# Kernel optimization log

Hardware: AMD Instinct MI355X
Metric: run time of the kernel (lower is better)

## Reference

```python
import jax, jax.numpy as jnp
import numpy as np

DIM = 768
NUM_SS = 8
INNER = DIM // 4  # s_ratio = 4 -> 192


def setup_inputs() -> dict:
    key = jax.random.key(0)
    ks = jax.random.split(key, 9)
    s = 0.02
    return {
        "x": jax.random.normal(ks[0], (16, 4096, DIM), dtype=jnp.float32),
        "Wq": jax.random.normal(ks[1], (DIM, DIM), dtype=jnp.float32) * s,
        "bq": jax.random.normal(ks[2], (DIM,), dtype=jnp.float32) * s,
        "Wk": jax.random.normal(ks[3], (DIM, NUM_SS * INNER), dtype=jnp.float32) * s,
        "bk": jax.random.normal(ks[4], (NUM_SS * INNER,), dtype=jnp.float32) * s,
        "Wv": jax.random.normal(ks[5], (DIM, DIM), dtype=jnp.float32) * s,
        "bv": jax.random.normal(ks[6], (DIM,), dtype=jnp.float32) * s,
        "Wss_out": jax.random.normal(ks[7], (INNER, DIM), dtype=jnp.float32) * s,
        "bss_out": jax.random.normal(ks[8], (DIM,), dtype=jnp.float32) * s,
    }


def reference(x, Wq, bq, Wk, bk, Wv, bv, Wss_out, bss_out):
    b = x.shape[0]
    ss_tokens = x[:, -NUM_SS:, :]          # [b, S, D]
    reg = x[:, :-NUM_SS, :]                # [b, T, D]
    x_v = reg @ Wv + bv                    # [b, T, D]
    x_q = reg @ Wq + bq                    # [b, T, D]
    x_k = reg @ Wk + bk                    # [b, T, S*I]
    # mean over regular tokens, reshape to one inner vector per ss token
    ss_update_ = jnp.mean(x_k, axis=1).reshape(b, NUM_SS, INNER)
    new_ss = ss_tokens + (ss_update_ @ Wss_out + bss_out)     # [b, S, D]
    scale = jnp.asarray(1.0 / np.sqrt(DIM), x.dtype)
    sim = jnp.einsum('btd,bsd->bts', x_q, new_ss) * scale     # [b, T, S]
    attn = jax.nn.softmax(sim, axis=-1)
    upd = jnp.einsum('bts,bsd->btd', attn, new_ss)            # [b, T, D]
    new_reg = jax.nn.relu(x_v + upd)
    return jnp.concatenate([new_reg, new_ss], axis=1)
```

## Files before the change

kernel.cpp:

```cpp
#include <hip/hip_runtime.h>
#include <hip/hip_bf16.h>

#define B_ 16
#define T_ 4096
#define TREG 4088
#define D_ 768
#define NSS 8
#define INNER_ 192
#define NK 1536

typedef unsigned int u32;
typedef unsigned short u16;
typedef __attribute__((ext_vector_type(8))) short bf16x8;
typedef __attribute__((ext_vector_type(4))) float f32x4;

__device__ __forceinline__ u16 f2bf(float f) {
  union { __hip_bfloat16 h; u16 u; } cv;
  cv.h = __float2bfloat16(f);
  return cv.u;
}

__device__ __forceinline__ void load16_lds(const void* g, void* l) {
  __builtin_amdgcn_global_load_lds(
      (const __attribute__((address_space(1))) u32*)(unsigned long long)g,
      (__attribute__((address_space(3))) u32*)(u32)(unsigned long long)l,
      16, 0, 0);
}

__global__ __launch_bounds__(256) void k_wvt(const float* __restrict__ Wv,
                                             u16* __restrict__ wvT) {
  __shared__ float tile[16][17];
  int tx = threadIdx.x & 15, ty = threadIdx.x >> 4;
  int nb = blockIdx.x * 16, kb = blockIdx.y * 16;
  tile[ty][tx] = Wv[(size_t)(kb + ty) * D_ + nb + tx];
  __syncthreads();
  wvT[(size_t)(nb + ty) * D_ + kb + tx] = f2bf(tile[tx][ty]);
}

template <bool CONV>
__global__ __launch_bounds__(192) void k_conv_mean(const float* __restrict__ x,
                                                   u16* __restrict__ xb,
                                                   float* __restrict__ means) {
  int b = blockIdx.y, tc = blockIdx.x, tid = threadIdx.x;
  const float4* xp = (const float4*)(x + (size_t)(b * T_ + tc * 128) * D_) + tid;
  ushort4* op = nullptr;
  if (CONV) op = ((ushort4*)(xb + (size_t)(b * T_ + tc * 128) * D_)) + tid;
  float s0 = 0, s1 = 0, s2 = 0, s3 = 0;
  int tbase = tc * 128;
  for (int tt = 0; tt < 128; ++tt) {
    float4 v = xp[(size_t)tt * 192];
    if (CONV) {
      ushort4 o;
      o.x = f2bf(v.x); o.y = f2bf(v.y); o.z = f2bf(v.z); o.w = f2bf(v.w);
      op[(size_t)tt * 192] = o;
    }
    if (tbase + tt < TREG) { s0 += v.x; s1 += v.y; s2 += v.z; s3 += v.w; }
  }
  float* m = means + (size_t)b * D_ + tid * 4;
  atomicAdd(m + 0, s0); atomicAdd(m + 1, s1);
  atomicAdd(m + 2, s2); atomicAdd(m + 3, s3);
}

__global__ __launch_bounds__(256) void k_ssu(const float* __restrict__ means,
                                             const float* __restrict__ Wk,
                                             const float* __restrict__ bk,
                                             float* __restrict__ ssu) {
  int b = blockIdx.y, tid = threadIdx.x;
  int n = blockIdx.x * 256 + tid;
  __shared__ float mv[D_];
  for (int d = tid; d < D_; d += 256)
    mv[d] = means[(size_t)b * D_ + d] * (1.0f / TREG);
  __syncthreads();
  float a = bk[n];
#pragma unroll 8
  for (int d = 0; d < D_; ++d) a += mv[d] * Wk[(size_t)d * NK + n];
  ssu[(size_t)b * NK + n] = a;
}

__global__ __launch_bounds__(256) void k_nss(
    const float* __restrict__ x, const float* __restrict__ ssu,
    const float* __restrict__ Wss, const float* __restrict__ bss,
    const float* __restrict__ bq, float* __restrict__ out,
    float* __restrict__ nssf, u16* __restrict__ nssT, float* __restrict__ qb) {
  int s = blockIdx.x, b = blockIdx.y, tid = threadIdx.x;
  __shared__ float su[INNER_];
  __shared__ float qred[4];
  if (tid < INNER_) su[tid] = ssu[(size_t)b * NK + s * INNER_ + tid];
  __syncthreads();
  size_t xr = (size_t)(b * T_ + TREG + s) * D_;
  float a0 = x[xr + tid]       + bss[tid];
  float a1 = x[xr + tid + 256] + bss[tid + 256];
  float a2 = x[xr + tid + 512] + bss[tid + 512];
#pragma unroll 4
  for (int i = 0; i < INNER_; ++i) {
    float sv = su[i];
    const float* wr = Wss + (size_t)i * D_ + tid;
    a0 += sv * wr[0]; a1 += sv * wr[256]; a2 += sv * wr[512];
  }
  out[xr + tid] = a0; out[xr + tid + 256] = a1; out[xr + tid + 512] = a2;
  size_t nb = (size_t)(b * NSS + s) * D_;
  nssf[nb + tid] = a0; nssf[nb + tid + 256] = a1; nssf[nb + tid + 512] = a2;
  size_t tb = (size_t)b * D_;
  nssT[(tb + tid) * NSS + s] = f2bf(a0);
  nssT[(tb + tid + 256) * NSS + s] = f2bf(a1);
  nssT[(tb + tid + 512) * NSS + s] = f2bf(a2);
  float q = bq[tid] * a0 + bq[tid + 256] * a1 + bq[tid + 512] * a2;
#pragma unroll
  for (int o = 1; o < 64; o <<= 1) q += __shfl_xor(q, o, 64);
  if ((tid & 63) == 0) qred[tid >> 6] = q;
  __syncthreads();
  if (tid == 0) qb[b * NSS + s] = qred[0] + qred[1] + qred[2] + qred[3];
}

__global__ __launch_bounds__(256) void k_wqs(const float* __restrict__ Wq,
                                             const float* __restrict__ nssf,
                                             u16* __restrict__ wqsT) {
  __shared__ float nss[NSS * (D_ + 4)];
  int b = blockIdx.y, tid = threadIdx.x;
  int o = blockIdx.x * 256 + tid;
  int j = o >> 3, s = o & 7;
  for (int i = tid; i < NSS * D_; i += 256) {
    int s2 = i / D_, d2 = i - s2 * D_;
    nss[s2 * (D_ + 4) + d2] = nssf[(size_t)b * NSS * D_ + i];
  }
  __syncthreads();
  const float* wr = Wq + (size_t)j * D_;
  const float* nr = nss + s * (D_ + 4);
  float a = 0;
#pragma unroll 8
  for (int d = 0; d < D_; ++d) a += wr[d] * nr[d];
  wqsT[((size_t)b * NSS + s) * D_ + j] = f2bf(a);
}

template <bool ABF16>
__global__ __launch_bounds__(256) void k_main(
    const u16* __restrict__ xb, const float* __restrict__ xf,
    const u16* __restrict__ wvT, const u16* __restrict__ wqsT,
    const u16* __restrict__ nssTg, const float* __restrict__ qb,
    const float* __restrict__ bv, float* __restrict__ out) {
  __shared__ uint4 ldsv[1800];
  u16* lds = (u16*)ldsv;
  u16* As = lds;
  u16* Bs = lds + 4096;
  u16* Ws = lds + 8192;

  const int tid = threadIdx.x;
  const int b = blockIdx.z;
  const int t0 = blockIdx.y * 128, n0 = blockIdx.x * 128;
  const int wave = tid >> 6, lane = tid & 63;
  const int wy = wave >> 1, wx = wave & 1;
  const int lr = lane & 15, lq = lane >> 4;

  if (tid < 96) {
    for (int s = 0; s < 8; ++s)
      ((uint4*)(Ws + s * 776))[tid] =
          ((const uint4*)(wqsT + ((size_t)b * NSS + s) * D_))[tid];
  }

  f32x4 acc[4][4];
  f32x4 sacc[4];
#pragma unroll
  for (int i = 0; i < 4; ++i) {
    sacc[i] = f32x4{0.f, 0.f, 0.f, 0.f};
#pragma unroll
    for (int j = 0; j < 4; ++j) acc[i][j] = f32x4{0.f, 0.f, 0.f, 0.f};
  }

  const u16* Bg = wvT + (size_t)n0 * D_;
  const int c1 = tid + 256;
  const int ar0 = tid >> 2, ak0 = (tid & 3) * 8;
  const int ar1 = c1 >> 2, ak1 = (c1 & 3) * 8;

  for (int k0 = 0; k0 < D_; k0 += 32) {
    if constexpr (ABF16) {
      const u16* Ag = xb + (size_t)(b * T_ + t0) * D_;
      load16_lds(Ag + (size_t)ar0 * D_ + k0 + ak0, As + tid * 8);
      load16_lds(Ag + (size_t)ar1 * D_ + k0 + ak1, As + c1 * 8);
    } else {
      const float* Af = xf + (size_t)(b * T_ + t0) * D_;
      const float* p0 = Af + (size_t)ar0 * D_ + k0 + ak0;
      const float* p1 = Af + (size_t)ar1 * D_ + k0 + ak1;
      float4 a0 = *(const float4*)p0, a1 = *(const float4*)(p0 + 4);
      float4 a2 = *(const float4*)p1, a3 = *(const float4*)(p1 + 4);
      ushort4 w0, w1, w2, w3;
      w0.x = f2bf(a0.x); w0.y = f2bf(a0.y); w0.z = f2bf(a0.z); w0.w = f2bf(a0.w);
      w1.x = f2bf(a1.x); w1.y = f2bf(a1.y); w1.z = f2bf(a1.z); w1.w = f2bf(a1.w);
      w2.x = f2bf(a2.x); w2.y = f2bf(a2.y); w2.z = f2bf(a2.z); w2.w = f2bf(a2.w);
      w3.x = f2bf(a3.x); w3.y = f2bf(a3.y); w3.z = f2bf(a3.z); w3.w = f2bf(a3.w);
      *(ushort4*)(As + tid * 8) = w0; *(ushort4*)(As + tid * 8 + 4) = w1;
      *(ushort4*)(As + c1 * 8) = w2; *(ushort4*)(As + c1 * 8 + 4) = w3;
    }
    load16_lds(Bg + (size_t)ar0 * D_ + k0 + ak0, Bs + tid * 8);
    load16_lds(Bg + (size_t)ar1 * D_ + k0 + ak1, Bs + c1 * 8);
    __syncthreads();

    bf16x8 af[4], bfr[4], qf;
#pragma unroll
    for (int mt = 0; mt < 4; ++mt)
      af[mt] = *(const bf16x8*)(As + (wy * 64 + mt * 16 + lr) * 32 + lq * 8);
#pragma unroll
    for (int nt = 0; nt < 4; ++nt)
      bfr[nt] = *(const bf16x8*)(Bs + (wx * 64 + nt * 16 + lr) * 32 + lq * 8);
    qf = *(const bf16x8*)(Ws + (lr & 7) * 776 + k0 + lq * 8);
#pragma unroll
    for (int mt = 0; mt < 4; ++mt) {
#pragma unroll
      for (int nt = 0; nt < 4; ++nt)
        acc[mt][nt] = __builtin_amdgcn_mfma_f32_16x16x32_bf16(
            af[mt], bfr[nt], acc[mt][nt], 0, 0, 0);
      sacc[mt] = __builtin_amdgcn_mfma_f32_16x16x32_bf16(
          af[mt], qf, sacc[mt], 0, 0, 0);
    }
    __syncthreads();
  }

  u16* anb = lds;
  u16* nsl = lds + 4096;
  {
    uint4 z; z.x = z.y = z.z = z.w = 0;
    if (tid < 128) {
      uint4 v = *(const uint4*)(nssTg + ((size_t)b * D_ + n0 + tid) * NSS);
      *(uint4*)(nsl + tid * 32) = v;
      *(uint4*)(nsl + tid * 32 + 8) = z;
      *(uint4*)(nsl + tid * 32 + 16) = z;
      *(uint4*)(nsl + tid * 32 + 24) = z;
    } else {
      int r = tid - 128;
      *(uint4*)(anb + r * 32 + 8) = z;
      *(uint4*)(anb + r * 32 + 16) = z;
      *(uint4*)(anb + r * 32 + 24) = z;
    }
  }
  __syncthreads();

  const float scale = 0.03608439182435161f;
  const float qbias = (lr < 8) ? qb[b * NSS + lr] : 0.f;
#pragma unroll
  for (int mt = 0; mt < 4; ++mt) {
    f32x4 s4 = sacc[mt];
#pragma unroll
    for (int r = 0; r < 4; ++r) {
      float v = (lr < 8) ? (s4[r] + qbias) * scale : -1.0e30f;
      float mx = v;
      mx = fmaxf(mx, __shfl_xor(mx, 1, 16));
      mx = fmaxf(mx, __shfl_xor(mx, 2, 16));
      mx = fmaxf(mx, __shfl_xor(mx, 4, 16));
      float e = (lr < 8) ? __expf(v - mx) : 0.f;
      float sm = e;
      sm += __shfl_xor(sm, 1, 16);
      sm += __shfl_xor(sm, 2, 16);
      sm += __shfl_xor(sm, 4, 16);
      if (lr < 8) {
        float a = e / sm;
        anb[(wy * 64 + mt * 16 + lq * 4 + r) * 32 + lr] = f2bf(a);
      }
    }
  }
  __syncthreads();

  bf16x8 nf[4];
#pragma unroll
  for (int nt = 0; nt < 4; ++nt)
    nf[nt] = *(const bf16x8*)(nsl + (wx * 64 + nt * 16 + lr) * 32 + lq * 8);
#pragma unroll
  for (int mt = 0; mt < 4; ++mt) {
    bf16x8 afr = *(const bf16x8*)(anb + (wy * 64 + mt * 16 + lr) * 32 + lq * 8);
#pragma unroll
    for (int nt = 0; nt < 4; ++nt)
      acc[mt][nt] = __builtin_amdgcn_mfma_f32_16x16x32_bf16(
          afr, nf[nt], acc[mt][nt], 0, 0, 0);
  }

  float bvv[4];
#pragma unroll
  for (int nt = 0; nt < 4; ++nt) bvv[nt] = bv[n0 + wx * 64 + nt * 16 + lr];
#pragma unroll
  for (int mt = 0; mt < 4; ++mt) {
    int trow = wy * 64 + mt * 16 + lq * 4;
#pragma unroll
    for (int r = 0; r < 4; ++r) {
      int token = t0 + trow + r;
      if (token < TREG) {
        float* op = out + ((size_t)b * T_ + token) * D_ + n0 + wx * 64;
#pragma unroll
        for (int nt = 0; nt < 4; ++nt)
          op[nt * 16 + lr] = fmaxf(acc[mt][nt][r] + bvv[nt], 0.f);
      }
    }
  }
}

extern "C" void kernel_launch(void* const* d_in, const int* in_sizes, int n_in,
                              void* d_out, int out_size, void* d_ws, size_t ws_size,
                              hipStream_t stream) {
  (void)in_sizes; (void)n_in; (void)out_size;
  const float* x   = (const float*)d_in[0];
  const float* Wq  = (const float*)d_in[1];
  const float* bq  = (const float*)d_in[2];
  const float* Wk  = (const float*)d_in[3];
  const float* bk  = (const float*)d_in[4];
  const float* Wv  = (const float*)d_in[5];
  const float* bv  = (const float*)d_in[6];
  const float* Wss = (const float*)d_in[7];
  const float* bss = (const float*)d_in[8];
  float* out = (float*)d_out;

  const size_t SZ_XB   = (size_t)B_ * T_ * D_ * 2;
  const size_t SZ_WVT  = (size_t)D_ * D_ * 2;
  const size_t SZ_MEAN = (size_t)B_ * D_ * 4;
  const size_t SZ_SSU  = (size_t)B_ * NK * 4;
  const size_t SZ_NSSF = (size_t)B_ * NSS * D_ * 4;
  const size_t SZ_NSST = (size_t)B_ * D_ * NSS * 2;
  const size_t SZ_QB   = (size_t)B_ * NSS * 4;
  const size_t SZ_WQS  = (size_t)B_ * NSS * D_ * 2;
  const size_t SMALL = SZ_WVT + SZ_MEAN + SZ_SSU + SZ_NSSF + SZ_NSST + SZ_QB + SZ_WQS;
  const size_t FULL = SZ_XB + SMALL;
  const bool big = ws_size >= FULL;

  char* ws = (char*)d_ws;
  size_t off = big ? SZ_XB : 0;
  u16*   xb    = (u16*)ws;
  u16*   wvT   = (u16*)(ws + off);   off += SZ_WVT;
  float* means = (float*)(ws + off); off += SZ_MEAN;
  float* ssu   = (float*)(ws + off); off += SZ_SSU;
  float* nssf  = (float*)(ws + off); off += SZ_NSSF;
  u16*   nssT  = (u16*)(ws + off);   off += SZ_NSST;
  float* qbb   = (float*)(ws + off); off += SZ_QB;
  u16*   wqsT  = (u16*)(ws + off);   off += SZ_WQS;

  hipMemsetAsync(means, 0, SZ_MEAN, stream);
  k_wvt<<<dim3(48, 48), 256, 0, stream>>>(Wv, wvT);
  if (big)
    k_conv_mean<true><<<dim3(32, 16), 192, 0, stream>>>(x, xb, means);
  else
    k_conv_mean<false><<<dim3(32, 16), 192, 0, stream>>>(x, nullptr, means);
  k_ssu<<<dim3(6, 16), 256, 0, stream>>>(means, Wk, bk, ssu);
  k_nss<<<dim3(NSS, 16), 256, 0, stream>>>(x, ssu, Wss, bss, bq, out, nssf, nssT, qbb);
  k_wqs<<<dim3(24, 16), 256, 0, stream>>>(Wq, nssf, wqsT);
  if (big)
    k_main<true><<<dim3(6, 32, 16), 256, 0, stream>>>(xb, x, wvT, wqsT, nssT, qbb, bv, out);
  else
    k_main<false><<<dim3(6, 32, 16), 256, 0, stream>>>(nullptr, x, wvT, wqsT, nssT, qbb, bv, out);
}
```

Baseline: 641.0 us.

## Load MFMA fragments directly from global with register prefetch, XCD-aware block swizzle

The main GEMM stops staging the A and B tiles through LDS and instead loads bf16 fragments straight from global memory into registers. It double-buffers them across k-steps and removes the per-iteration barriers. The 1D grid is remapped so that blocks sharing an x tile land on the same XCD for L2 reuse, and launch bounds request 3 blocks per CU with a smaller LDS footprint. The conversion and mean kernel is also split into 4x more blocks for more parallelism, at the cost of 4x more atomics. Direct global fragment loads are less coalesced than LDS staging and raise register pressure.

```diff
diff --git a/kernel.cpp b/kernel.cpp
--- a/kernel.cpp
+++ b/kernel.cpp
@@ -20,13 +20,6 @@
   return cv.u;
 }
 
-__device__ __forceinline__ void load16_lds(const void* g, void* l) {
-  __builtin_amdgcn_global_load_lds(
-      (const __attribute__((address_space(1))) u32*)(unsigned long long)g,
-      (__attribute__((address_space(3))) u32*)(u32)(unsigned long long)l,
-      16, 0, 0);
-}
-
 __global__ __launch_bounds__(256) void k_wvt(const float* __restrict__ Wv,
                                              u16* __restrict__ wvT) {
   __shared__ float tile[16][17];
@@ -42,12 +35,13 @@
                                                    u16* __restrict__ xb,
                                                    float* __restrict__ means) {
   int b = blockIdx.y, tc = blockIdx.x, tid = threadIdx.x;
-  const float4* xp = (const float4*)(x + (size_t)(b * T_ + tc * 128) * D_) + tid;
+  const float4* xp = (const float4*)(x + (size_t)(b * T_ + tc * 32) * D_) + tid;
   ushort4* op = nullptr;
-  if (CONV) op = ((ushort4*)(xb + (size_t)(b * T_ + tc * 128) * D_)) + tid;
+  if (CONV) op = ((ushort4*)(xb + (size_t)(b * T_ + tc * 32) * D_)) + tid;
   float s0 = 0, s1 = 0, s2 = 0, s3 = 0;
-  int tbase = tc * 128;
-  for (int tt = 0; tt < 128; ++tt) {
+  int tbase = tc * 32;
+#pragma unroll 4
+  for (int tt = 0; tt < 32; ++tt) {
     float4 v = xp[(size_t)tt * 192];
     if (CONV) {
       ushort4 o;
@@ -132,21 +126,44 @@
   wqsT[((size_t)b * NSS + s) * D_ + j] = f2bf(a);
 }
 
+template <bool BF>
+__device__ __forceinline__ bf16x8 ldfrag(const u16* pb, const float* pf,
+                                         size_t off) {
+  if constexpr (BF) {
+    return *(const bf16x8*)(pb + off);
+  } else {
+    float4 f0 = *(const float4*)(pf + off);
+    float4 f1 = *(const float4*)(pf + off + 4);
+    bf16x8 r;
+    r[0] = (short)f2bf(f0.x); r[1] = (short)f2bf(f0.y);
+    r[2] = (short)f2bf(f0.z); r[3] = (short)f2bf(f0.w);
+    r[4] = (short)f2bf(f1.x); r[5] = (short)f2bf(f1.y);
+    r[6] = (short)f2bf(f1.z); r[7] = (short)f2bf(f1.w);
+    return r;
+  }
+}
+
 template <bool ABF16>
-__global__ __launch_bounds__(256) void k_main(
+__global__ __launch_bounds__(256, 3) void k_main(
     const u16* __restrict__ xb, const float* __restrict__ xf,
     const u16* __restrict__ wvT, const u16* __restrict__ wqsT,
     const u16* __restrict__ nssTg, const float* __restrict__ qb,
     const float* __restrict__ bv, float* __restrict__ out) {
-  __shared__ uint4 ldsv[1800];
+  __shared__ uint4 ldsv[1024];
   u16* lds = (u16*)ldsv;
-  u16* As = lds;
-  u16* Bs = lds + 4096;
-  u16* Ws = lds + 8192;
+  u16* Ws = lds;
 
   const int tid = threadIdx.x;
-  const int b = blockIdx.z;
-  const int t0 = blockIdx.y * 128, n0 = blockIdx.x * 128;
+  const int g = blockIdx.x;
+  const int xcd = g & 7;
+  const int li = g >> 3;
+  const int nblk = li % 6;
+  const int pair = li / 6;
+  const int pid = pair * 8 + xcd;
+  const int t0 = (pid & 31) * 128;
+  const int b = pid >> 5;
+  const int n0 = nblk * 128;
+
   const int wave = tid >> 6, lane = tid & 63;
   const int wy = wave >> 1, wx = wave & 1;
   const int lr = lane & 15, lq = lane >> 4;
@@ -156,6 +173,7 @@
       ((uint4*)(Ws + s * 776))[tid] =
           ((const uint4*)(wqsT + ((size_t)b * NSS + s) * D_))[tid];
   }
+  __syncthreads();
 
   f32x4 acc[4][4];
   f32x4 sacc[4];
@@ -166,54 +184,46 @@
     for (int j = 0; j < 4; ++j) acc[i][j] = f32x4{0.f, 0.f, 0.f, 0.f};
   }
 
-  const u16* Bg = wvT + (size_t)n0 * D_;
-  const int c1 = tid + 256;
-  const int ar0 = tid >> 2, ak0 = (tid & 3) * 8;
-  const int ar1 = c1 >> 2, ak1 = (c1 & 3) * 8;
-
-  for (int k0 = 0; k0 < D_; k0 += 32) {
-    if constexpr (ABF16) {
-      const u16* Ag = xb + (size_t)(b * T_ + t0) * D_;
-      load16_lds(Ag + (size_t)ar0 * D_ + k0 + ak0, As + tid * 8);
-      load16_lds(Ag + (size_t)ar1 * D_ + k0 + ak1, As + c1 * 8);
-    } else {
-      const float* Af = xf + (size_t)(b * T_ + t0) * D_;
-      const float* p0 = Af + (size_t)ar0 * D_ + k0 + ak0;
-      const float* p1 = Af + (size_t)ar1 * D_ + k0 + ak1;
-      float4 a0 = *(const float4*)p0, a1 = *(const float4*)(p0 + 4);
-      float4 a2 = *(const float4*)p1, a3 = *(const float4*)(p1 + 4);
-      ushort4 w0, w1, w2, w3;
-      w0.x = f2bf(a0.x); w0.y = f2bf(a0.y); w0.z = f2bf(a0.z); w0.w = f2bf(a0.w);
-      w1.x = f2bf(a1.x); w1.y = f2bf(a1.y); w1.z = f2bf(a1.z); w1.w = f2bf(a1.w);
-      w2.x = f2bf(a2.x); w2.y = f2bf(a2.y); w2.z = f2bf(a2.z); w2.w = f2bf(a2.w);
-      w3.x = f2bf(a3.x); w3.y = f2bf(a3.y); w3.z = f2bf(a3.z); w3.w = f2bf(a3.w);
-      *(ushort4*)(As + tid * 8) = w0; *(ushort4*)(As + tid * 8 + 4) = w1;
-      *(ushort4*)(As + c1 * 8) = w2; *(ushort4*)(As + c1 * 8 + 4) = w3;
-    }
-    load16_lds(Bg + (size_t)ar0 * D_ + k0 + ak0, Bs + tid * 8);
-    load16_lds(Bg + (size_t)ar1 * D_ + k0 + ak1, Bs + c1 * 8);
-    __syncthreads();
-
-    bf16x8 af[4], bfr[4], qf;
-#pragma unroll
-    for (int mt = 0; mt < 4; ++mt)
-      af[mt] = *(const bf16x8*)(As + (wy * 64 + mt * 16 + lr) * 32 + lq * 8);
-#pragma unroll
-    for (int nt = 0; nt < 4; ++nt)
-      bfr[nt] = *(const bf16x8*)(Bs + (wx * 64 + nt * 16 + lr) * 32 + lq * 8);
-    qf = *(const bf16x8*)(Ws + (lr & 7) * 776 + k0 + lq * 8);
+  const u16* Ab = ABF16 ? xb + (size_t)(b * T_ + t0 + wy * 64) * D_ + lq * 8
+                        : nullptr;
+  const float* Af = ABF16 ? nullptr
+                          : xf + (size_t)(b * T_ + t0 + wy * 64) * D_ + lq * 8;
+  const u16* Bb = wvT + (size_t)(n0 + wx * 64) * D_ + lq * 8;
+
+  bf16x8 aC[4], bC[4], aN[4], bN[4];
+#pragma unroll
+  for (int mt = 0; mt < 4; ++mt)
+    aC[mt] = ldfrag<ABF16>(Ab, Af, (size_t)(mt * 16 + lr) * D_);
+#pragma unroll
+  for (int nt = 0; nt < 4; ++nt)
+    bC[nt] = *(const bf16x8*)(Bb + (size_t)(nt * 16 + lr) * D_);
+
+#pragma unroll
+  for (int kk = 0; kk < 24; ++kk) {
+    const int k0 = kk * 32;
+    if (kk < 23) {
+#pragma unroll
+      for (int mt = 0; mt < 4; ++mt)
+        aN[mt] = ldfrag<ABF16>(Ab, Af, (size_t)(mt * 16 + lr) * D_ + k0 + 32);
+#pragma unroll
+      for (int nt = 0; nt < 4; ++nt)
+        bN[nt] = *(const bf16x8*)(Bb + (size_t)(nt * 16 + lr) * D_ + k0 + 32);
+    }
+    bf16x8 qf = *(const bf16x8*)(Ws + (lr & 7) * 776 + k0 + lq * 8);
 #pragma unroll
     for (int mt = 0; mt < 4; ++mt) {
 #pragma unroll
       for (int nt = 0; nt < 4; ++nt)
         acc[mt][nt] = __builtin_amdgcn_mfma_f32_16x16x32_bf16(
-            af[mt], bfr[nt], acc[mt][nt], 0, 0, 0);
+            aC[mt], bC[nt], acc[mt][nt], 0, 0, 0);
       sacc[mt] = __builtin_amdgcn_mfma_f32_16x16x32_bf16(
-          af[mt], qf, sacc[mt], 0, 0, 0);
-    }
-    __syncthreads();
-  }
-
+          aC[mt], qf, sacc[mt], 0, 0, 0);
+    }
+#pragma unroll
+    for (int i = 0; i < 4; ++i) { aC[i] = aN[i]; bC[i] = bN[i]; }
+  }
+
+  __syncthreads();
   u16* anb = lds;
   u16* nsl = lds + 4096;
   {
@@ -331,14 +341,14 @@
   hipMemsetAsync(means, 0, SZ_MEAN, stream);
   k_wvt<<<dim3(48, 48), 256, 0, stream>>>(Wv, wvT);
   if (big)
-    k_conv_mean<true><<<dim3(32, 16), 192, 0, stream>>>(x, xb, means);
+    k_conv_mean<true><<<dim3(128, 16), 192, 0, stream>>>(x, xb, means);
   else
-    k_conv_mean<false><<<dim3(32, 16), 192, 0, stream>>>(x, nullptr, means);
+    k_conv_mean<false><<<dim3(128, 16), 192, 0, stream>>>(x, nullptr, means);
   k_ssu<<<dim3(6, 16), 256, 0, stream>>>(means, Wk, bk, ssu);
   k_nss<<<dim3(NSS, 16), 256, 0, stream>>>(x, ssu, Wss, bss, bq, out, nssf, nssT, qbb);
   k_wqs<<<dim3(24, 16), 256, 0, stream>>>(Wq, nssf, wqsT);
   if (big)
-    k_main<true><<<dim3(6, 32, 16), 256, 0, stream>>>(xb, x, wvT, wqsT, nssT, qbb, bv, out);
+    k_main<true><<<3072, 256, 0, stream>>>(xb, x, wvT, wqsT, nssT, qbb, bv, out);
   else
-    k_main<false><<<dim3(6, 32, 16), 256, 0, stream>>>(nullptr, x, wvT, wqsT, nssT, qbb, bv, out);
-}
+    k_main<false><<<3072, 256, 0, stream>>>(nullptr, x, wvT, wqsT, nssT, qbb, bv, out);
+}
```

Result: slower. 757.7 us (+18.2%).

## Split conv-mean into more chunks, drop atomics, remap main grid per XCD

Applied to the files above, without the earlier changes.

The column-sum kernel now uses 128 chunks of 32 tokens instead of 32 chunks of 128, which raises parallelism for the bandwidth-bound fp32-to-bf16 conversion pass. Each chunk writes partial sums to workspace, replacing the float atomics and the memset, and the ssu kernel reduces those partials. The main GEMM launches as a flat 1D grid and remaps block IDs so that the six N-tiles of one row tile land on the same XCD, so the shared A tile gets reused in that XCD's L2. It also adds a launch-bounds occupancy hint of 3 blocks per SM, which costs a larger partials buffer and possible register pressure.

```diff
diff --git a/kernel.cpp b/kernel.cpp
--- a/kernel.cpp
+++ b/kernel.cpp
@@ -8,6 +8,7 @@
 #define NSS 8
 #define INNER_ 192
 #define NK 1536
+#define NCHUNK 128
 
 typedef unsigned int u32;
 typedef unsigned short u16;
@@ -40,14 +41,15 @@
 template <bool CONV>
 __global__ __launch_bounds__(192) void k_conv_mean(const float* __restrict__ x,
                                                    u16* __restrict__ xb,
-                                                   float* __restrict__ means) {
+                                                   float* __restrict__ partials) {
   int b = blockIdx.y, tc = blockIdx.x, tid = threadIdx.x;
-  const float4* xp = (const float4*)(x + (size_t)(b * T_ + tc * 128) * D_) + tid;
+  const float4* xp = (const float4*)(x + (size_t)(b * T_ + tc * 32) * D_) + tid;
   ushort4* op = nullptr;
-  if (CONV) op = ((ushort4*)(xb + (size_t)(b * T_ + tc * 128) * D_)) + tid;
+  if (CONV) op = ((ushort4*)(xb + (size_t)(b * T_ + tc * 32) * D_)) + tid;
   float s0 = 0, s1 = 0, s2 = 0, s3 = 0;
-  int tbase = tc * 128;
-  for (int tt = 0; tt < 128; ++tt) {
+  int tbase = tc * 32;
+#pragma unroll 4
+  for (int tt = 0; tt < 32; ++tt) {
     float4 v = xp[(size_t)tt * 192];
     if (CONV) {
       ushort4 o;
@@ -56,20 +58,24 @@
     }
     if (tbase + tt < TREG) { s0 += v.x; s1 += v.y; s2 += v.z; s3 += v.w; }
   }
-  float* m = means + (size_t)b * D_ + tid * 4;
-  atomicAdd(m + 0, s0); atomicAdd(m + 1, s1);
-  atomicAdd(m + 2, s2); atomicAdd(m + 3, s3);
-}
-
-__global__ __launch_bounds__(256) void k_ssu(const float* __restrict__ means,
+  float4 st; st.x = s0; st.y = s1; st.z = s2; st.w = s3;
+  ((float4*)(partials + ((size_t)b * NCHUNK + tc) * D_))[tid] = st;
+}
+
+__global__ __launch_bounds__(256) void k_ssu(const float* __restrict__ partials,
                                              const float* __restrict__ Wk,
                                              const float* __restrict__ bk,
                                              float* __restrict__ ssu) {
   int b = blockIdx.y, tid = threadIdx.x;
   int n = blockIdx.x * 256 + tid;
   __shared__ float mv[D_];
-  for (int d = tid; d < D_; d += 256)
-    mv[d] = means[(size_t)b * D_ + d] * (1.0f / TREG);
+  for (int d = tid; d < D_; d += 256) {
+    const float* p = partials + (size_t)b * NCHUNK * D_ + d;
+    float s = 0;
+#pragma unroll 8
+    for (int c = 0; c < NCHUNK; ++c) s += p[(size_t)c * D_];
+    mv[d] = s * (1.0f / TREG);
+  }
   __syncthreads();
   float a = bk[n];
 #pragma unroll 8
@@ -133,7 +139,7 @@
 }
 
 template <bool ABF16>
-__global__ __launch_bounds__(256) void k_main(
+__global__ __launch_bounds__(256, 3) void k_main(
     const u16* __restrict__ xb, const float* __restrict__ xf,
     const u16* __restrict__ wvT, const u16* __restrict__ wqsT,
     const u16* __restrict__ nssTg, const float* __restrict__ qb,
@@ -145,8 +151,16 @@
   u16* Ws = lds + 8192;
 
   const int tid = threadIdx.x;
-  const int b = blockIdx.z;
-  const int t0 = blockIdx.y * 128, n0 = blockIdx.x * 128;
+  const int g = blockIdx.x;
+  const int xcd = g & 7;
+  const int li = g >> 3;
+  const int nblk = li % 6;
+  const int pair = li / 6;
+  const int pid = pair * 8 + xcd;
+  const int t0 = (pid & 31) * 128;
+  const int b = pid >> 5;
+  const int n0 = nblk * 128;
+
   const int wave = tid >> 6, lane = tid & 63;
   const int wy = wave >> 1, wx = wave & 1;
   const int lr = lane & 15, lq = lane >> 4;
@@ -307,13 +321,13 @@
 
   const size_t SZ_XB   = (size_t)B_ * T_ * D_ * 2;
   const size_t SZ_WVT  = (size_t)D_ * D_ * 2;
-  const size_t SZ_MEAN = (size_t)B_ * D_ * 4;
+  const size_t SZ_PART = (size_t)B_ * NCHUNK * D_ * 4;
   const size_t SZ_SSU  = (size_t)B_ * NK * 4;
   const size_t SZ_NSSF = (size_t)B_ * NSS * D_ * 4;
   const size_t SZ_NSST = (size_t)B_ * D_ * NSS * 2;
   const size_t SZ_QB   = (size_t)B_ * NSS * 4;
   const size_t SZ_WQS  = (size_t)B_ * NSS * D_ * 2;
-  const size_t SMALL = SZ_WVT + SZ_MEAN + SZ_SSU + SZ_NSSF + SZ_NSST + SZ_QB + SZ_WQS;
+  const size_t SMALL = SZ_WVT + SZ_PART + SZ_SSU + SZ_NSSF + SZ_NSST + SZ_QB + SZ_WQS;
   const size_t FULL = SZ_XB + SMALL;
   const bool big = ws_size >= FULL;
 
@@ -321,24 +335,23 @@
   size_t off = big ? SZ_XB : 0;
   u16*   xb    = (u16*)ws;
   u16*   wvT   = (u16*)(ws + off);   off += SZ_WVT;
-  float* means = (float*)(ws + off); off += SZ_MEAN;
+  float* parts = (float*)(ws + off); off += SZ_PART;
   float* ssu   = (float*)(ws + off); off += SZ_SSU;
   float* nssf  = (float*)(ws + off); off += SZ_NSSF;
   u16*   nssT  = (u16*)(ws + off);   off += SZ_NSST;
   float* qbb   = (float*)(ws + off); off += SZ_QB;
   u16*   wqsT  = (u16*)(ws + off);   off += SZ_WQS;
 
-  hipMemsetAsync(means, 0, SZ_MEAN, stream);
   k_wvt<<<dim3(48, 48), 256, 0, stream>>>(Wv, wvT);
   if (big)
-    k_conv_mean<true><<<dim3(32, 16), 192, 0, stream>>>(x, xb, means);
+    k_conv_mean<true><<<dim3(NCHUNK, 16), 192, 0, stream>>>(x, xb, parts);
   else
-    k_conv_mean<false><<<dim3(32, 16), 192, 0, stream>>>(x, nullptr, means);
-  k_ssu<<<dim3(6, 16), 256, 0, stream>>>(means, Wk, bk, ssu);
+    k_conv_mean<false><<<dim3(NCHUNK, 16), 192, 0, stream>>>(x, nullptr, parts);
+  k_ssu<<<dim3(6, 16), 256, 0, stream>>>(parts, Wk, bk, ssu);
   k_nss<<<dim3(NSS, 16), 256, 0, stream>>>(x, ssu, Wss, bss, bq, out, nssf, nssT, qbb);
   k_wqs<<<dim3(24, 16), 256, 0, stream>>>(Wq, nssf, wqsT);
   if (big)
-    k_main<true><<<dim3(6, 32, 16), 256, 0, stream>>>(xb, x, wvT, wqsT, nssT, qbb, bv, out);
+    k_main<true><<<3072, 256, 0, stream>>>(xb, x, wvT, wqsT, nssT, qbb, bv, out);
   else
-    k_main<false><<<dim3(6, 32, 16), 256, 0, stream>>>(nullptr, x, wvT, wqsT, nssT, qbb, bv, out);
-}
+    k_main<false><<<3072, 256, 0, stream>>>(nullptr, x, wvT, wqsT, nssT, qbb, bv, out);
+}
```

New measurement: 606.2 us. 5.4% less time.
